# Performance work log

Measured on AMD Instinct MI355X. Metric: run time of the kernel, lower is better.

Reference implementation:

```python
import jax, jax.numpy as jnp
import numpy as np

NUM_BINS = 256          # CLAHE histogram bins (kornia default)
GRID = (8, 8)           # CLAHE tile grid (kornia default)
LOG_GAIN = 2.5          # module init arg
CLIP_LIMIT = 1.0        # module init arg


def normalize_in_range(x, lo=0.0, hi=1.0):
    mn = x.min()
    mx = x.max()
    return (x - mn) / (mx - mn) * (hi - lo) + lo


def adjust_log(x, gain):
    # skimage/kornia log adjust: gain * log2(1 + x)
    return gain * jnp.log2(1.0 + x)


def equalize_clahe(x, clip_limit=CLIP_LIMIT, grid=GRID):
    B, C, H, W = x.shape
    gh, gw = grid
    th = -(-H // gh)   # ceil tile height
    tw = -(-W // gw)   # ceil tile width
    Hp, Wp = th * gh, tw * gw
    if (Hp, Wp) != (H, W):
        x = jnp.pad(x, ((0, 0), (0, 0), (0, Hp - H), (0, Wp - W)), mode='reflect')

    # bin index per pixel (values saturated into [0,1])
    xc = jnp.clip(x, 0.0, 1.0)
    bins = jnp.clip((xc * NUM_BINS).astype(jnp.int32), 0, NUM_BINS - 1)  # B,C,Hp,Wp

    # --- per-tile histograms: (B*C*gh*gw) tiles of th*tw pixels ---
    tb = bins.reshape(B, C, gh, th, gw, tw).transpose(0, 1, 2, 4, 3, 5)
    tb = tb.reshape(B * C * gh * gw, th * tw)
    hist = jax.vmap(lambda ix: jnp.bincount(ix, length=NUM_BINS))(tb).astype(jnp.float32)

    pixels = th * tw
    # --- clip + uniform redistribution of excess ---
    if clip_limit > 0:
        clip_max = max(int(clip_limit * pixels // NUM_BINS), 1)
        excess = jnp.maximum(hist - clip_max, 0.0).sum(-1)
        hist = jnp.minimum(hist, float(clip_max))
        redist = jnp.floor(excess / NUM_BINS)
        residual = excess - redist * NUM_BINS
        hist = hist + redist[:, None] \
             + (jnp.arange(NUM_BINS)[None, :] < residual[:, None]).astype(hist.dtype)

    # --- CDF -> LUT in [0, 255] ---
    lut = jnp.clip(jnp.floor(jnp.cumsum(hist, -1) * ((NUM_BINS - 1) / pixels)), 0.0, NUM_BINS - 1.0)
    lut = lut.reshape(B, C, gh, gw, NUM_BINS)

    # --- bilinear interpolation between the 4 neighboring tile LUTs ---
    iy = jnp.arange(Hp, dtype=jnp.float32)
    ty = (iy + 0.5) / th - 0.5
    y0f = jnp.floor(ty)
    wy = (ty - y0f)[:, None]                                   # Hp x 1
    y0 = jnp.clip(y0f.astype(jnp.int32), 0, gh - 1)[:, None]
    y1 = jnp.clip(y0f.astype(jnp.int32) + 1, 0, gh - 1)[:, None]

    ix = jnp.arange(Wp, dtype=jnp.float32)
    tx = (ix + 0.5) / tw - 0.5
    x0f = jnp.floor(tx)
    wx = (tx - x0f)[None, :]
    x0 = jnp.clip(x0f.astype(jnp.int32), 0, gw - 1)[None, :]
    x1 = jnp.clip(x0f.astype(jnp.int32) + 1, 0, gw - 1)[None, :]

    flat_lut = lut.reshape(-1)
    bidx = jnp.arange(B)[:, None, None, None]
    cidx = jnp.arange(C)[None, :, None, None]

    def gather(yi, xi):
        idx = (((bidx * C + cidx) * gh + yi) * gw + xi) * NUM_BINS + bins
        return flat_lut[idx]

    v = (1.0 - wy) * ((1.0 - wx) * gather(y0, x0) + wx * gather(y0, x1)) \
        + wy * ((1.0 - wx) * gather(y1, x0) + wx * gather(y1, x1))
    out = v / (NUM_BINS - 1)
    return out[..., :H, :W]


def setup_inputs() -> dict:
    key = jax.random.key(0)
    x = jax.random.uniform(key, (8, 1, 2048, 2048), dtype=jnp.float32)
    return {"x": x}


def reference(x):
    shape = x.shape
    x = normalize_in_range(x, 0.0, 1.0)
    x = adjust_log(x, gain=LOG_GAIN)
    x = equalize_clahe(x, clip_limit=CLIP_LIMIT)
    x = normalize_in_range(x, 0.0, 1.0)
    return x.reshape(shape)
```

## Files before the change

### kernel.cpp

```cpp
#include <hip/hip_runtime.h>

#define NIMG 8
#define IMH 2048
#define IMW 2048
#define GH 8
#define GW 8
#define NBINS 256
#define NTPI 64
#define CLIP_MAXF 256.0f
#define LUT_SCALE 0.0038909912109375f
#define LOG_GAIN_F 2.5f

#define MM_BLOCKS 2048

typedef float f32x4 __attribute__((ext_vector_type(4)));

__device__ __forceinline__ int pix_bin(float v, float mn, float inv_den) {
    float xn = (v - mn) * inv_den;
    float t  = LOG_GAIN_F * __log2f(1.0f + xn);
    float xc = fminf(fmaxf(t, 0.0f), 1.0f);
    int b = (int)(xc * 256.0f);
    return min(max(b, 0), 255);
}

__device__ __forceinline__ void mm4(float4 v, float& mn, float& mx) {
    mn = fminf(mn, fminf(fminf(v.x, v.y), fminf(v.z, v.w)));
    mx = fmaxf(mx, fmaxf(fmaxf(v.x, v.y), fmaxf(v.z, v.w)));
}

template <int NWAVES>
__device__ __forceinline__ void block_minmax_all(float& mn, float& mx, int t) {
#pragma unroll
    for (int m = 32; m >= 1; m >>= 1) {
        mn = fminf(mn, __shfl_xor(mn, m, 64));
        mx = fmaxf(mx, __shfl_xor(mx, m, 64));
    }
    __shared__ float smn[NWAVES], smx[NWAVES];
    int wid = t >> 6, lid = t & 63;
    if (lid == 0) { smn[wid] = mn; smx[wid] = mx; }
    __syncthreads();
    mn = smn[0]; mx = smx[0];
#pragma unroll
    for (int i = 1; i < NWAVES; i++) { mn = fminf(mn, smn[i]); mx = fmaxf(mx, smx[i]); }
}

__global__ __launch_bounds__(256) void k_minmax_in(const float4* __restrict__ x,
                                                   float2* __restrict__ red) {
    int t = threadIdx.x;
    size_t base = (size_t)blockIdx.x * 4096 + t;
    float mn = 3.4e38f, mx = -3.4e38f;
#pragma unroll
    for (int half = 0; half < 2; ++half) {
        float4 v[8];
#pragma unroll
        for (int k = 0; k < 8; ++k)
            v[k] = x[base + (size_t)(half * 8 + k) * 256];
#pragma unroll
        for (int k = 0; k < 8; ++k) mm4(v[k], mn, mx);
    }
    block_minmax_all<4>(mn, mx, t);
    if (t == 0) red[blockIdx.x] = make_float2(mn, mx);
}

__global__ __launch_bounds__(1024) void k_hist(const float* __restrict__ x,
                                               const float2* __restrict__ red1,
                                               float* __restrict__ lut,
                                               uchar4* __restrict__ bins) {
    int t = threadIdx.x;

    float mn, mx;
    {
        float2 p0 = red1[t];
        float2 p1 = red1[t + 1024];
        mn = fminf(p0.x, p1.x);
        mx = fmaxf(p0.y, p1.y);
        block_minmax_all<16>(mn, mx, t);
    }
    float inv_den = 1.0f / (mx - mn);

    __shared__ unsigned sh[NBINS];
    if (t < NBINS) sh[t] = 0u;
    __syncthreads();

    int tile = blockIdx.x;
    int img  = blockIdx.y;
    int ty = tile >> 3, tx = tile & 7;

    size_t base = ((size_t)img * IMH + (size_t)ty * 256) * IMW + (size_t)tx * 256;
    const float* xt = x + base;
    int lid = t & 63;
    int rowoff = t >> 6;
    int c4 = t & 63;

    int hotcnt = 0;
    for (int it = 0; it < 16; it += 2) {
        int r0 = (it << 4) + rowoff;
        int r1 = ((it + 1) << 4) + rowoff;
        float4 va = *(const float4*)(xt + (size_t)r0 * IMW + (c4 << 2));
        float4 vb = *(const float4*)(xt + (size_t)r1 * IMW + (c4 << 2));

        int ba[4], bb[4];
        ba[0] = pix_bin(va.x, mn, inv_den); ba[1] = pix_bin(va.y, mn, inv_den);
        ba[2] = pix_bin(va.z, mn, inv_den); ba[3] = pix_bin(va.w, mn, inv_den);
        bb[0] = pix_bin(vb.x, mn, inv_den); bb[1] = pix_bin(vb.y, mn, inv_den);
        bb[2] = pix_bin(vb.z, mn, inv_den); bb[3] = pix_bin(vb.w, mn, inv_den);

#pragma unroll
        for (int j = 0; j < 4; j++) {
            hotcnt += (ba[j] == 255);
            if (ba[j] != 255) atomicAdd(&sh[ba[j]], 1u);
            hotcnt += (bb[j] == 255);
            if (bb[j] != 255) atomicAdd(&sh[bb[j]], 1u);
        }
        uchar4 qa, qb;
        qa.x = (unsigned char)ba[0]; qa.y = (unsigned char)ba[1];
        qa.z = (unsigned char)ba[2]; qa.w = (unsigned char)ba[3];
        qb.x = (unsigned char)bb[0]; qb.y = (unsigned char)bb[1];
        qb.z = (unsigned char)bb[2]; qb.w = (unsigned char)bb[3];
        bins[(base + (size_t)r0 * IMW + (size_t)(c4 << 2)) >> 2] = qa;
        bins[(base + (size_t)r1 * IMW + (size_t)(c4 << 2)) >> 2] = qb;
    }
#pragma unroll
    for (int m = 1; m < 64; m <<= 1) hotcnt += __shfl_xor(hotcnt, m, 64);
    if (lid == 0 && hotcnt) atomicAdd(&sh[255], (unsigned)hotcnt);
    __syncthreads();

    int wid = t >> 6;
    float h = 0.0f, ex = 0.0f;
    if (t < NBINS) {
        h = (float)sh[t];
        ex = fmaxf(h - CLIP_MAXF, 0.0f);
    }
    float s = ex;
#pragma unroll
    for (int m = 1; m < 64; m <<= 1) s += __shfl_xor(s, m, 64);
    __shared__ float wpart[16];
    if (lid == 0) wpart[wid] = s;
    __syncthreads();
    float excess = wpart[0] + wpart[1] + wpart[2] + wpart[3];

    h = fminf(h, CLIP_MAXF);
    float redist   = floorf(excess * (1.0f / 256.0f));
    float residual = excess - redist * 256.0f;
    h = h + redist + (((float)t < residual) ? 1.0f : 0.0f);

    float c = h;
#pragma unroll
    for (int m = 1; m < 64; m <<= 1) {
        float o = __shfl_up(c, m, 64);
        if (lid >= m) c += o;
    }
    __shared__ float wsum[16];
    if (lid == 63) wsum[wid] = c;
    __syncthreads();
    if (t < NBINS) {
        float off = 0.0f;
        for (int i = 0; i < wid; i++) off += wsum[i];
        c += off;
        float l = fminf(floorf(c * LUT_SCALE), 255.0f);
        l = fmaxf(l, 0.0f);
        lut[((size_t)img * NTPI + tile) * NBINS + t] = l;
    }
}

template <bool FINAL>
__global__ __launch_bounds__(256) void k_apply(const uchar4* __restrict__ bins,
                                               const float* __restrict__ lut,
                                               float2* __restrict__ red2,
                                               float4* __restrict__ out) {
    __shared__ float4 Lq[NBINS];
    int t = threadIdx.x;

    float s1 = 1.0f, s2 = 0.0f;
    if (FINAL) {
        float vmn = 3.4e38f, vmx = -3.4e38f;
#pragma unroll
        for (int k = 0; k < 8; k++) {
            float2 p = red2[t + k * 256];
            vmn = fminf(vmn, p.x);
            vmx = fmaxf(vmx, p.y);
        }
        block_minmax_all<4>(vmn, vmx, t);
        float pmn = vmn * (1.0f / 255.0f);
        float pmx = vmx * (1.0f / 255.0f);
        float oscale = 1.0f / (pmx - pmn);
        s1 = oscale * (1.0f / 255.0f);
        s2 = -pmn * oscale;
    }

    int qx = blockIdx.x, qy = blockIdx.y, img = blockIdx.z;
    const float* lb = lut + (size_t)img * NTPI * NBINS;
    {
        int ty2 = qy >> 1, tx2 = qx >> 1;
        int yA = (qy & 1) ? ty2 : max(ty2 - 1, 0);
        int yB = (qy & 1) ? min(ty2 + 1, GH - 1) : ty2;
        int xA = (qx & 1) ? tx2 : max(tx2 - 1, 0);
        int xB = (qx & 1) ? min(tx2 + 1, GW - 1) : tx2;
        float4 g;
        g.x = lb[(size_t)(yA * GW + xA) * NBINS + t] * s1 + s2;
        g.y = lb[(size_t)(yA * GW + xB) * NBINS + t] * s1 + s2;
        g.z = lb[(size_t)(yB * GW + xA) * NBINS + t] * s1 + s2;
        g.w = lb[(size_t)(yB * GW + xB) * NBINS + t] * s1 + s2;
        Lq[t] = g;
    }
    __syncthreads();

    float vmnl = 3.4e38f, vmxl = -3.4e38f;
    int gy0 = qy << 7, gx0 = qx << 7;
    int rowoff = t >> 5;
    int c4 = t & 31;
    int ix0 = gx0 + (c4 << 2);

    float wxv[4];
#pragma unroll
    for (int j = 0; j < 4; j++) {
        float txf = ((float)(ix0 + j) + 0.5f) * (1.0f / 256.0f) - 0.5f;
        wxv[j] = txf - floorf(txf);
    }

    for (int it = 0; it < 16; it += 2) {
        int r0 = (it << 3) + rowoff;
        int r1 = ((it + 1) << 3) + rowoff;
        int iy0 = gy0 + r0, iy1 = gy0 + r1;
        size_t p0 = ((size_t)img * IMH + iy0) * IMW + ix0;
        size_t p1 = ((size_t)img * IMH + iy1) * IMW + ix0;
        uchar4 qa = bins[p0 >> 2];
        uchar4 qb = bins[p1 >> 2];

#pragma unroll
        for (int half = 0; half < 2; ++half) {
            uchar4 q = half ? qb : qa;
            int iy = half ? iy1 : iy0;
            size_t pidx = half ? p1 : p0;
            int b[4] = {q.x, q.y, q.z, q.w};
            float tyf = ((float)iy + 0.5f) * (1.0f / 256.0f) - 0.5f;
            float wy = tyf - floorf(tyf);
            float4 o;
            float* op = &o.x;
#pragma unroll
            for (int j = 0; j < 4; j++) {
                float4 g = Lq[b[j]];
                float a = g.x + wxv[j] * (g.y - g.x);
                float bbv = g.z + wxv[j] * (g.w - g.z);
                float v = a + wy * (bbv - a);
                if (FINAL) {
                    op[j] = v;
                } else {
                    vmnl = fminf(vmnl, v);
                    vmxl = fmaxf(vmxl, v);
                }
            }
            if (FINAL) {
                f32x4 ov = {o.x, o.y, o.z, o.w};
                __builtin_nontemporal_store(ov, (f32x4*)&out[pidx >> 2]);
            }
        }
    }

    if (!FINAL) {
        block_minmax_all<4>(vmnl, vmxl, t);
        if (t == 0) {
            int bid = (img * 16 + qy) * 16 + qx;
            red2[bid] = make_float2(vmnl, vmxl);
        }
    }
}

extern "C" void kernel_launch(void* const* d_in, const int* in_sizes, int n_in,
                              void* d_out, int out_size, void* d_ws, size_t ws_size,
                              hipStream_t stream) {
    const float* x = (const float*)d_in[0];
    float4* out = (float4*)d_out;

    unsigned char* ws = (unsigned char*)d_ws;
    float* lut    = (float*)(ws + 64);
    float2* red1  = (float2*)(ws + 64 + 512 * 1024);
    float2* red2  = (float2*)(ws + 64 + 512 * 1024 + 16384);
    uchar4* bins  = (uchar4*)(ws + 1024 * 1024);

    k_minmax_in<<<dim3(MM_BLOCKS), dim3(256), 0, stream>>>((const float4*)x, red1);
    k_hist<<<dim3(NTPI, NIMG), dim3(1024), 0, stream>>>(x, red1, lut, bins);
    dim3 qgrid(16, 16, NIMG);
    k_apply<false><<<qgrid, dim3(256), 0, stream>>>(bins, lut, red2, out);
    k_apply<true><<<qgrid, dim3(256), 0, stream>>>(bins, lut, red2, out);
}
```

Before: 106.0 us.

## Store bins in quadrant-contiguous layout, drop max reduction, shrink histogram blocks

The 8-bit bin image is now written in a layout where each 128x128 quadrant is contiguous, so the apply kernels read one linear block instead of strided rows. The second min/max pass becomes a min-only pass, since the max pixel always maps to LUT value 255 and the output max is then fixed at 1. The histogram kernel moves from 1024-thread to 512-thread blocks with more iterations each, and occupancy hints are added to the launch bounds. The scattered quadrant stores in the histogram kernel add address arithmetic and may coalesce less well.

```diff
diff --git a/kernel.cpp b/kernel.cpp
--- a/kernel.cpp
+++ b/kernel.cpp
@@ -44,8 +44,21 @@
     for (int i = 1; i < NWAVES; i++) { mn = fminf(mn, smn[i]); mx = fmaxf(mx, smx[i]); }
 }
 
-__global__ __launch_bounds__(256) void k_minmax_in(const float4* __restrict__ x,
-                                                   float2* __restrict__ red) {
+template <int NWAVES>
+__device__ __forceinline__ void block_min_all(float& mn, int t) {
+#pragma unroll
+    for (int m = 32; m >= 1; m >>= 1) mn = fminf(mn, __shfl_xor(mn, m, 64));
+    __shared__ float smn[NWAVES];
+    int wid = t >> 6, lid = t & 63;
+    if (lid == 0) smn[wid] = mn;
+    __syncthreads();
+    mn = smn[0];
+#pragma unroll
+    for (int i = 1; i < NWAVES; i++) mn = fminf(mn, smn[i]);
+}
+
+__global__ __launch_bounds__(256, 8) void k_minmax_in(const float4* __restrict__ x,
+                                                      float2* __restrict__ red) {
     int t = threadIdx.x;
     size_t base = (size_t)blockIdx.x * 4096 + t;
     float mn = 3.4e38f, mx = -3.4e38f;
@@ -62,19 +75,21 @@
     if (t == 0) red[blockIdx.x] = make_float2(mn, mx);
 }
 
-__global__ __launch_bounds__(1024) void k_hist(const float* __restrict__ x,
-                                               const float2* __restrict__ red1,
-                                               float* __restrict__ lut,
-                                               uchar4* __restrict__ bins) {
+__global__ __launch_bounds__(512, 4) void k_hist(const float* __restrict__ x,
+                                                 const float2* __restrict__ red1,
+                                                 float* __restrict__ lut,
+                                                 uchar4* __restrict__ binsq) {
     int t = threadIdx.x;
 
     float mn, mx;
     {
         float2 p0 = red1[t];
-        float2 p1 = red1[t + 1024];
-        mn = fminf(p0.x, p1.x);
-        mx = fmaxf(p0.y, p1.y);
-        block_minmax_all<16>(mn, mx, t);
+        float2 p1 = red1[t + 512];
+        float2 p2 = red1[t + 1024];
+        float2 p3 = red1[t + 1536];
+        mn = fminf(fminf(p0.x, p1.x), fminf(p2.x, p3.x));
+        mx = fmaxf(fmaxf(p0.y, p1.y), fmaxf(p2.y, p3.y));
+        block_minmax_all<8>(mn, mx, t);
     }
     float inv_den = 1.0f / (mx - mn);
 
@@ -91,11 +106,14 @@
     int lid = t & 63;
     int rowoff = t >> 6;
     int c4 = t & 63;
+    int qc = c4 >> 5;
+    int gq_base = img * 256 + (2 * ty) * 16 + (2 * tx) + qc;
+    int qoff_c = c4 & 31;
 
     int hotcnt = 0;
-    for (int it = 0; it < 16; it += 2) {
+    for (int it = 0; it < 16; ++it) {
         int r0 = (it << 4) + rowoff;
-        int r1 = ((it + 1) << 4) + rowoff;
+        int r1 = (it << 4) + 8 + rowoff;
         float4 va = *(const float4*)(xt + (size_t)r0 * IMW + (c4 << 2));
         float4 vb = *(const float4*)(xt + (size_t)r1 * IMW + (c4 << 2));
 
@@ -117,8 +135,10 @@
         qa.z = (unsigned char)ba[2]; qa.w = (unsigned char)ba[3];
         qb.x = (unsigned char)bb[0]; qb.y = (unsigned char)bb[1];
         qb.z = (unsigned char)bb[2]; qb.w = (unsigned char)bb[3];
-        bins[(base + (size_t)r0 * IMW + (size_t)(c4 << 2)) >> 2] = qa;
-        bins[(base + (size_t)r1 * IMW + (size_t)(c4 << 2)) >> 2] = qb;
+        int gq0 = gq_base + ((r0 >> 7) << 4);
+        int gq1 = gq_base + ((r1 >> 7) << 4);
+        binsq[(size_t)gq0 * 4096 + ((r0 & 127) << 5) + qoff_c] = qa;
+        binsq[(size_t)gq1 * 4096 + ((r1 & 127) << 5) + qoff_c] = qb;
     }
 #pragma unroll
     for (int m = 1; m < 64; m <<= 1) hotcnt += __shfl_xor(hotcnt, m, 64);
@@ -134,7 +154,7 @@
     float s = ex;
 #pragma unroll
     for (int m = 1; m < 64; m <<= 1) s += __shfl_xor(s, m, 64);
-    __shared__ float wpart[16];
+    __shared__ float wpart[8];
     if (lid == 0) wpart[wid] = s;
     __syncthreads();
     float excess = wpart[0] + wpart[1] + wpart[2] + wpart[3];
@@ -150,7 +170,7 @@
         float o = __shfl_up(c, m, 64);
         if (lid >= m) c += o;
     }
-    __shared__ float wsum[16];
+    __shared__ float wsum[8];
     if (lid == 63) wsum[wid] = c;
     __syncthreads();
     if (t < NBINS) {
@@ -163,27 +183,86 @@
     }
 }
 
-template <bool FINAL>
-__global__ __launch_bounds__(256) void k_apply(const uchar4* __restrict__ bins,
-                                               const float* __restrict__ lut,
-                                               float2* __restrict__ red2,
-                                               float4* __restrict__ out) {
+
+__global__ __launch_bounds__(256, 8) void k_vmin(const uchar4* __restrict__ binsq,
+                                                 const float* __restrict__ lut,
+                                                 float* __restrict__ red2) {
     __shared__ float4 Lq[NBINS];
     int t = threadIdx.x;
-
-    float s1 = 1.0f, s2 = 0.0f;
-    if (FINAL) {
-        float vmn = 3.4e38f, vmx = -3.4e38f;
-#pragma unroll
-        for (int k = 0; k < 8; k++) {
-            float2 p = red2[t + k * 256];
-            vmn = fminf(vmn, p.x);
-            vmx = fmaxf(vmx, p.y);
+    int qx = blockIdx.x, qy = blockIdx.y, img = blockIdx.z;
+    const float* lb = lut + (size_t)img * NTPI * NBINS;
+    {
+        int ty2 = qy >> 1, tx2 = qx >> 1;
+        int yA = (qy & 1) ? ty2 : max(ty2 - 1, 0);
+        int yB = (qy & 1) ? min(ty2 + 1, GH - 1) : ty2;
+        int xA = (qx & 1) ? tx2 : max(tx2 - 1, 0);
+        int xB = (qx & 1) ? min(tx2 + 1, GW - 1) : tx2;
+        float4 g;
+        g.x = lb[(size_t)(yA * GW + xA) * NBINS + t];
+        g.y = lb[(size_t)(yA * GW + xB) * NBINS + t];
+        g.z = lb[(size_t)(yB * GW + xA) * NBINS + t];
+        g.w = lb[(size_t)(yB * GW + xB) * NBINS + t];
+        Lq[t] = g;
+    }
+    __syncthreads();
+
+    int gq = (img * 16 + qy) * 16 + qx;
+    const uchar4* bq = binsq + (size_t)gq * 4096;
+
+    float vmnl = 3.4e38f;
+    int gy0 = qy << 7, gx0 = qx << 7;
+    int rowoff = t >> 5;
+    int c4 = t & 31;
+    int ix0 = gx0 + (c4 << 2);
+
+    float wxv[4];
+#pragma unroll
+    for (int j = 0; j < 4; j++) {
+        float txf = ((float)(ix0 + j) + 0.5f) * (1.0f / 256.0f) - 0.5f;
+        wxv[j] = txf - floorf(txf);
+    }
+
+    for (int it = 0; it < 16; it += 2) {
+        int r0 = (it << 3) + rowoff;
+        int r1 = ((it + 1) << 3) + rowoff;
+        uchar4 qa = bq[(r0 << 5) + c4];
+        uchar4 qb = bq[(r1 << 5) + c4];
+#pragma unroll
+        for (int half = 0; half < 2; ++half) {
+            uchar4 q = half ? qb : qa;
+            int r = half ? r1 : r0;
+            int iy = gy0 + r;
+            int b[4] = {q.x, q.y, q.z, q.w};
+            float tyf = ((float)iy + 0.5f) * (1.0f / 256.0f) - 0.5f;
+            float wy = tyf - floorf(tyf);
+#pragma unroll
+            for (int j = 0; j < 4; j++) {
+                float4 g = Lq[b[j]];
+                float a = g.x + wxv[j] * (g.y - g.x);
+                float bbv = g.z + wxv[j] * (g.w - g.z);
+                vmnl = fminf(vmnl, a + wy * (bbv - a));
+            }
         }
-        block_minmax_all<4>(vmn, vmx, t);
+    }
+    block_min_all<4>(vmnl, t);
+    if (t == 0) red2[gq] = vmnl;
+}
+
+__global__ __launch_bounds__(256, 8) void k_final(const uchar4* __restrict__ binsq,
+                                                  const float* __restrict__ lut,
+                                                  const float* __restrict__ red2,
+                                                  float4* __restrict__ out) {
+    __shared__ float4 Lq[NBINS];
+    int t = threadIdx.x;
+
+    float s1, s2;
+    {
+        float vmn = 3.4e38f;
+#pragma unroll
+        for (int k = 0; k < 8; k++) vmn = fminf(vmn, red2[t + k * 256]);
+        block_min_all<4>(vmn, t);
         float pmn = vmn * (1.0f / 255.0f);
-        float pmx = vmx * (1.0f / 255.0f);
-        float oscale = 1.0f / (pmx - pmn);
+        float oscale = 1.0f / (1.0f - pmn);
         s1 = oscale * (1.0f / 255.0f);
         s2 = -pmn * oscale;
     }
@@ -205,7 +284,9 @@
     }
     __syncthreads();
 
-    float vmnl = 3.4e38f, vmxl = -3.4e38f;
+    int gq = (img * 16 + qy) * 16 + qx;
+    const uchar4* bq = binsq + (size_t)gq * 4096;
+
     int gy0 = qy << 7, gx0 = qx << 7;
     int rowoff = t >> 5;
     int c4 = t & 31;
@@ -221,17 +302,13 @@
     for (int it = 0; it < 16; it += 2) {
         int r0 = (it << 3) + rowoff;
         int r1 = ((it + 1) << 3) + rowoff;
-        int iy0 = gy0 + r0, iy1 = gy0 + r1;
-        size_t p0 = ((size_t)img * IMH + iy0) * IMW + ix0;
-        size_t p1 = ((size_t)img * IMH + iy1) * IMW + ix0;
-        uchar4 qa = bins[p0 >> 2];
-        uchar4 qb = bins[p1 >> 2];
-
+        uchar4 qa = bq[(r0 << 5) + c4];
+        uchar4 qb = bq[(r1 << 5) + c4];
 #pragma unroll
         for (int half = 0; half < 2; ++half) {
             uchar4 q = half ? qb : qa;
-            int iy = half ? iy1 : iy0;
-            size_t pidx = half ? p1 : p0;
+            int r = half ? r1 : r0;
+            int iy = gy0 + r;
             int b[4] = {q.x, q.y, q.z, q.w};
             float tyf = ((float)iy + 0.5f) * (1.0f / 256.0f) - 0.5f;
             float wy = tyf - floorf(tyf);
@@ -242,26 +319,11 @@
                 float4 g = Lq[b[j]];
                 float a = g.x + wxv[j] * (g.y - g.x);
                 float bbv = g.z + wxv[j] * (g.w - g.z);
-                float v = a + wy * (bbv - a);
-                if (FINAL) {
-                    op[j] = v;
-                } else {
-                    vmnl = fminf(vmnl, v);
-                    vmxl = fmaxf(vmxl, v);
-                }
+                op[j] = a + wy * (bbv - a);
             }
-            if (FINAL) {
-                f32x4 ov = {o.x, o.y, o.z, o.w};
-                __builtin_nontemporal_store(ov, (f32x4*)&out[pidx >> 2]);
-            }
-        }
-    }
-
-    if (!FINAL) {
-        block_minmax_all<4>(vmnl, vmxl, t);
-        if (t == 0) {
-            int bid = (img * 16 + qy) * 16 + qx;
-            red2[bid] = make_float2(vmnl, vmxl);
+            size_t pidx = ((size_t)img * IMH + iy) * IMW + ix0;
+            f32x4 ov = {o.x, o.y, o.z, o.w};
+            __builtin_nontemporal_store(ov, (f32x4*)&out[pidx >> 2]);
         }
     }
 }
@@ -275,12 +337,12 @@
     unsigned char* ws = (unsigned char*)d_ws;
     float* lut    = (float*)(ws + 64);
     float2* red1  = (float2*)(ws + 64 + 512 * 1024);
-    float2* red2  = (float2*)(ws + 64 + 512 * 1024 + 16384);
-    uchar4* bins  = (uchar4*)(ws + 1024 * 1024);
+    float* red2   = (float*)(ws + 64 + 512 * 1024 + 16384);
+    uchar4* binsq = (uchar4*)(ws + 1024 * 1024);
 
     k_minmax_in<<<dim3(MM_BLOCKS), dim3(256), 0, stream>>>((const float4*)x, red1);
-    k_hist<<<dim3(NTPI, NIMG), dim3(1024), 0, stream>>>(x, red1, lut, bins);
+    k_hist<<<dim3(NTPI, NIMG), dim3(512), 0, stream>>>(x, red1, lut, binsq);
     dim3 qgrid(16, 16, NIMG);
-    k_apply<false><<<qgrid, dim3(256), 0, stream>>>(bins, lut, red2, out);
-    k_apply<true><<<qgrid, dim3(256), 0, stream>>>(bins, lut, red2, out);
-}
+    k_vmin<<<qgrid, dim3(256), 0, stream>>>(binsq, lut, red2);
+    k_final<<<qgrid, dim3(256), 0, stream>>>(binsq, lut, red2, out);
+}
```

Measured after the change: 105.0 us. No clear change (-0.9%).
